# Optimization experiments

Hardware: AMD Instinct MI355X
Metric: run time of the kernel (lower is better)

## Reference

```python
import jax, jax.numpy as jnp
import numpy as np

B, S, H, W, C = 1, 42, 42, 42, 96
WS = 7            # window size (cubic)
SHIFT = 3         # cyclic shift
NH = 3            # num heads
HD = C // NH      # head dim = 32
N = WS ** 3       # tokens per window = 343
NW = (S // WS) * (H // WS) * (W // WS)  # 216 windows
SCALE = HD ** -0.5
EPS = 1e-5


def _rel_pos_index():
    # exact replica of the torch buffer construction (meshgrid 'ij')
    coords = np.stack(np.meshgrid(np.arange(WS), np.arange(WS), np.arange(WS), indexing='ij'))
    flat = coords.reshape(3, -1)                      # (3, N)
    rel = flat[:, :, None] - flat[:, None, :]          # (3, N, N)
    rel = rel.transpose(1, 2, 0).astype(np.int64)      # (N, N, 3)
    rel[..., 0] += WS - 1
    rel[..., 1] += WS - 1
    rel[..., 2] += WS - 1
    rel[..., 0] *= 3 * WS - 1
    rel[..., 1] *= 2 * WS - 1
    return jnp.asarray(rel.sum(-1))                    # (N, N) int

REL_IDX = _rel_pos_index()


def _layernorm(x, w, b):
    mu = jnp.mean(x, -1, keepdims=True)
    var = jnp.mean(jnp.square(x - mu), -1, keepdims=True)
    return (x - mu) * jax.lax.rsqrt(var + EPS) * w + b


def setup_inputs() -> dict:
    key = jax.random.key(0)
    ks = jax.random.split(key, 8)
    std = 0.02
    return {
        'x': jax.random.normal(ks[0], (B, S * H * W, C), jnp.float32),
        'mask_matrix': jnp.zeros((NW, N, N), jnp.float32),
        'norm1_w': jnp.ones((C,), jnp.float32),
        'norm1_b': jnp.zeros((C,), jnp.float32),
        'qkv_w': jax.random.normal(ks[1], (C, 3 * C), jnp.float32) * std,
        'qkv_b': jnp.zeros((3 * C,), jnp.float32),
        'proj_w': jax.random.normal(ks[2], (C, C), jnp.float32) * std,
        'proj_b': jnp.zeros((C,), jnp.float32),
        'rpb_table': jax.random.normal(ks[3], ((2 * WS - 1) ** 3, NH), jnp.float32) * std,
        'norm2_w': jnp.ones((C,), jnp.float32),
        'norm2_b': jnp.zeros((C,), jnp.float32),
        'fc1_w': jax.random.normal(ks[4], (C, 4 * C), jnp.float32) * std,
        'fc1_b': jnp.zeros((4 * C,), jnp.float32),
        'fc2_w': jax.random.normal(ks[5], (4 * C, C), jnp.float32) * std,
        'fc2_b': jnp.zeros((C,), jnp.float32),
    }


def _block(x, mask, norm1_w, norm1_b, qkv_w, qkv_b, proj_w, proj_b,
           rpb_table, norm2_w, norm2_b, fc1_w, fc1_b, fc2_w, fc2_b):
    shortcut = x
    h = _layernorm(x, norm1_w, norm1_b).reshape(B, S, H, W, C)
    # cyclic shift (S,H,W divisible by WS -> no padding needed)
    h = jnp.roll(h, shift=(-SHIFT, -SHIFT, -SHIFT), axis=(1, 2, 3))
    # window partition -> (B*nW, N, C)
    h = h.reshape(B, S // WS, WS, H // WS, WS, W // WS, WS, C)
    h = h.transpose(0, 1, 3, 5, 2, 4, 6, 7).reshape(-1, N, C)
    B_ = h.shape[0]  # B * NW
    # attention
    qkv = (h @ qkv_w + qkv_b).reshape(B_, N, 3, NH, HD).transpose(2, 0, 3, 1, 4)
    q, k, v = qkv[0] * SCALE, qkv[1], qkv[2]
    attn = jnp.einsum('bhnd,bhmd->bhnm', q, k)           # (B_, NH, N, N)
    bias = rpb_table[REL_IDX.reshape(-1)].reshape(N, N, NH).transpose(2, 0, 1)
    attn = attn + bias[None]
    attn = attn.reshape(B, NW, NH, N, N) + mask[None, :, None]
    attn = jax.nn.softmax(attn.reshape(B_, NH, N, N), axis=-1)
    out = jnp.einsum('bhnm,bhmd->bhnd', attn, v).transpose(0, 2, 1, 3).reshape(B_, N, C)
    out = out @ proj_w + proj_b
    # window reverse + reverse shift
    out = out.reshape(B, S // WS, H // WS, W // WS, WS, WS, WS, C)
    out = out.transpose(0, 1, 4, 2, 5, 3, 6, 7).reshape(B, S, H, W, C)
    out = jnp.roll(out, shift=(SHIFT, SHIFT, SHIFT), axis=(1, 2, 3)).reshape(B, S * H * W, C)
    x = shortcut + out
    # MLP with exact (erf) GELU, matching nn.GELU default
    m = _layernorm(x, norm2_w, norm2_b)
    m = jax.nn.gelu(m @ fc1_w + fc1_b, approximate=False) @ fc2_w + fc2_b
    return x + m


def reference(x, mask_matrix, norm1_w, norm1_b, qkv_w, qkv_b, proj_w, proj_b,
              rpb_table, norm2_w, norm2_b, fc1_w, fc1_b, fc2_w, fc2_b):
    return _block(x, mask_matrix, norm1_w, norm1_b, qkv_w, qkv_b, proj_w, proj_b,
                  rpb_table, norm2_w, norm2_b, fc1_w, fc1_b, fc2_w, fc2_b)
```

## Files before the change

### kernel.cpp

```cpp
#include <hip/hip_runtime.h>
#include <hip/hip_bf16.h>
#include <math.h>

#define SDIM 42
#define CDIM 96
#define NTOK 74088
#define NWIN 216
#define NSEQ 343
#define NTOT 7112448
#define QK_SCALE 0.17677669529663687f
#define LN_EPS 1e-5f

typedef short short8 __attribute__((ext_vector_type(8)));
typedef float f32x4 __attribute__((ext_vector_type(4)));
typedef unsigned eu4 __attribute__((ext_vector_type(4)));
union I4S8 { int4 i; short8 s; };

__device__ __forceinline__ int tok_index(int w, int n) {
    int wq = w / 36;
    int wrem = w - wq * 36;
    int wh = wrem / 6;
    int ww = wrem - wh * 6;
    int ps = n / 49;
    int prem = n - ps * 49;
    int ph = prem / 7;
    int pw = prem - ph * 7;
    int s = wq * 7 + ps + 3; if (s >= SDIM) s -= SDIM;
    int h = wh * 7 + ph + 3; if (h >= SDIM) h -= SDIM;
    int c = ww * 7 + pw + 3; if (c >= SDIM) c -= SDIM;
    return (s * SDIM + h) * SDIM + c;
}

__device__ __forceinline__ unsigned pk2(float a, float b) {
    unsigned ua = (unsigned)__bfloat16_as_ushort(__float2bfloat16(a));
    unsigned ub = (unsigned)__bfloat16_as_ushort(__float2bfloat16(b));
    return ua | (ub << 16);
}

__device__ __forceinline__ float fast_erf(float x) {
    float ax = fabsf(x);
    float t = 1.0f / (1.0f + 0.3275911f * ax);
    float y = t*(0.254829592f + t*(-0.284496736f +
              t*(1.421413741f + t*(-1.453152027f + t*1.061405429f))));
    float r = 1.0f - y * __expf(-ax*ax);
    return copysignf(r, x);
}
__device__ __forceinline__ float gelu(float v) {
    return 0.5f * v * (1.0f + fast_erf(v * 0.70710678118654752f));
}

__global__ __launch_bounds__(384) void k_wcast(
    const float* __restrict__ w1, const float* __restrict__ w2,
    const float* __restrict__ pw, const float* __restrict__ qkvw,
    __hip_bfloat16* __restrict__ w1t, __hip_bfloat16* __restrict__ w2t,
    __hip_bfloat16* __restrict__ pwt, __hip_bfloat16* __restrict__ qkvt)
{
    int b = blockIdx.x, t = threadIdx.x;
    if (b < 384) {
        if (t < 96) w1t[(size_t)b*96 + t] = __float2bfloat16(w1[(size_t)t*384 + b]);
    } else if (b < 480) {
        int r = b - 384;
        w2t[(size_t)r*384 + t] = __float2bfloat16(w2[(size_t)t*96 + r]);
    } else if (b < 576) {
        int r = b - 480;
        if (t < 96) pwt[(size_t)r*96 + t] = __float2bfloat16(pw[(size_t)t*96 + r]);
    } else {
        int c = b - 576;
        if (t < 96) qkvt[(size_t)c*96 + t] = __float2bfloat16(qkvw[(size_t)t*288 + c]);
    }
}

__global__ __launch_bounds__(256) void k_fused_prep(
    const float* __restrict__ x,
    const float* __restrict__ n1w, const float* __restrict__ n1b,
    const __hip_bfloat16* __restrict__ qkvt, const float* __restrict__ qkvb,
    __hip_bfloat16* __restrict__ qb, __hip_bfloat16* __restrict__ kb,
    __hip_bfloat16* __restrict__ vb,
    const float* __restrict__ mask, unsigned* __restrict__ mflag,
    const float* __restrict__ rpb, float* __restrict__ bg)
{
    __shared__ __align__(16) __hip_bfloat16 sX[64*104];
    __shared__ unsigned sFlag;
    const int b = blockIdx.x;
    const int tid = threadIdx.x;

    if (b >= 1296 + NWIN) {
        const int p = b - (1296 + NWIN);
        const int m = p % NSEQ, hh = p / NSEQ;
        const int a0 = m / 49, ar = m - a0*49, a1 = ar / 7, a2 = ar - a1*7;
        for (int n = tid; n < NSEQ; n += 256) {
            int b0 = n / 49, br = n - b0*49, b1 = br / 7, b2 = br - b1*7;
            int idx = (a0 - b0 + 6)*20 + (a1 - b1 + 6)*13 + (a2 - b2 + 6);
            bg[((size_t)hh*NSEQ + m)*NSEQ + n] = rpb[idx*3 + hh];
        }
        return;
    }
    if (b >= 1296) {
        const int w = b - 1296;
        if (tid == 0) sFlag = 0;
        __syncthreads();
        const unsigned* p = (const unsigned*)(mask + (size_t)w * NSEQ * NSEQ);
        unsigned acc = 0;
        const eu4* p4 = (const eu4*)p;
        for (int i = tid; i < (NSEQ*NSEQ)/4; i += 256) {
            eu4 v = __builtin_nontemporal_load(p4 + i);
            acc |= (v[0] << 1) | (v[1] << 1) | (v[2] << 1) | (v[3] << 1);
        }
        if (tid == 0) acc |= (p[NSEQ*NSEQ - 1] << 1);
        if (__any(acc != 0) && (tid & 63) == 0) atomicOr(&sFlag, 1u);
        __syncthreads();
        if (tid == 0) mflag[w] = sFlag;
        return;
    }

    const int w  = b / 6;
    const int n0 = (b - w*6) * 64;
    const int g = tid >> 5, l = tid & 31;
    {
        const float lw0 = n1w[l], lw1 = n1w[l+32], lw2 = n1w[l+64];
        const float lb0 = n1b[l], lb1 = n1b[l+32], lb2 = n1b[l+64];
        for (int rr = 0; rr < 8; ++rr) {
            int row = g * 8 + rr;
            int n = n0 + row;
            if (n < NSEQ) {
                const float* xr = x + (size_t)tok_index(w, n) * CDIM;
                float x0 = __builtin_nontemporal_load(xr + l);
                float x1 = __builtin_nontemporal_load(xr + l + 32);
                float x2 = __builtin_nontemporal_load(xr + l + 64);
                float s = x0 + x1 + x2;
                #pragma unroll
                for (int m = 16; m; m >>= 1) s += __shfl_xor(s, m, 32);
                float mu = s * (1.0f/96.0f);
                float d0 = x0-mu, d1 = x1-mu, d2 = x2-mu;
                float vv = d0*d0 + d1*d1 + d2*d2;
                #pragma unroll
                for (int m = 16; m; m >>= 1) vv += __shfl_xor(vv, m, 32);
                float rstd = rsqrtf(vv * (1.0f/96.0f) + LN_EPS);
                sX[row*104 + l]    = __float2bfloat16(d0 * rstd * lw0 + lb0);
                sX[row*104 + l+32] = __float2bfloat16(d1 * rstd * lw1 + lb1);
                sX[row*104 + l+64] = __float2bfloat16(d2 * rstd * lw2 + lb2);
            } else {
                sX[row*104 + l]    = __float2bfloat16(0.f);
                sX[row*104 + l+32] = __float2bfloat16(0.f);
                sX[row*104 + l+64] = __float2bfloat16(0.f);
            }
        }
    }
    __syncthreads();

    const int wv = tid >> 6, lane = tid & 63;
    const int l15 = lane & 15, h = lane >> 4;
    const int trow = wv*16 + l15;
    const int n = n0 + trow;

    I4S8 bx[3];
    #pragma unroll
    for (int ks = 0; ks < 3; ++ks)
        bx[ks].i = *(const int4*)&sX[trow*104 + ks*32 + h*8];

    for (int nt = 0; nt < 18; ++nt) {
        f32x4 acc = {0.f,0.f,0.f,0.f};
        #pragma unroll
        for (int ks = 0; ks < 3; ++ks) {
            I4S8 af;
            af.i = *(const int4*)(qkvt + (size_t)(nt*16 + l15)*96 + ks*32 + h*8);
            acc = __builtin_amdgcn_mfma_f32_16x16x32_bf16(af.s, bx[ks].s, acc, 0, 0, 0);
        }
        if (n < NSEQ) {
            const int colbase = nt*16 + 4*h;
            const int sel = colbase / 96;
            const int rem = colbase - sel*96;
            const int head = rem >> 5, d0 = rem & 31;
            float4 bb = *(const float4*)&qkvb[colbase];
            float v0 = acc[0] + bb.x, v1 = acc[1] + bb.y;
            float v2 = acc[2] + bb.z, v3 = acc[3] + bb.w;
            if (sel == 0) { v0 *= QK_SCALE; v1 *= QK_SCALE; v2 *= QK_SCALE; v3 *= QK_SCALE; }
            __hip_bfloat16* dst = (sel == 0 ? qb : (sel == 1 ? kb : vb));
            *(uint2*)&dst[(((size_t)w*3 + head)*NSEQ + n)*32 + d0] =
                make_uint2(pk2(v0, v1), pk2(v2, v3));
        }
    }
}

template<bool UM>
__device__ __forceinline__ void attn_qloop(
    const __hip_bfloat16* __restrict__ qb, const float* __restrict__ bg,
    const float* __restrict__ mask, __hip_bfloat16* __restrict__ aob,
    const __hip_bfloat16* sK, const __hip_bfloat16* sVT,
    size_t base, int w, int head, int wid, int l15, int h)
{
    for (int mt = wid; mt < 22; mt += 8) {
        const int m = mt*16 + l15;
        const int mc = (m < NSEQ) ? m : (NSEQ-1);

        I4S8 qf;
        qf.i = *(const int4*)(qb + base + (size_t)mc*32 + h*8);

        const float* mrow = mask + ((size_t)w*NSEQ + mc)*NSEQ;
        const float* brow = bg   + ((size_t)head*NSEQ + mc)*NSEQ;

        float lsum = 0.f;
        f32x4 acc0 = {0.f,0.f,0.f,0.f}, acc1 = {0.f,0.f,0.f,0.f};

        auto step = [&](int t, float4 mkA, float4 bsA, float4 mkB, float4 bsB) {
            float p[8];
            {
                I4S8 kf;
                kf.i = *(const int4*)&sK[(t*16 + l15)*32 + h*8];
                f32x4 st = __builtin_amdgcn_mfma_f32_16x16x32_bf16(
                    kf.s, qf.s, (f32x4){0.f,0.f,0.f,0.f}, 0, 0, 0);
                if constexpr (UM) {
                    p[0] = __expf(st[0] + mkA.x + bsA.x);
                    p[1] = __expf(st[1] + mkA.y + bsA.y);
                    p[2] = __expf(st[2] + mkA.z + bsA.z);
                    p[3] = __expf(st[3] + mkA.w + bsA.w);
                } else {
                    p[0] = __expf(st[0] + bsA.x);
                    p[1] = __expf(st[1] + bsA.y);
                    p[2] = __expf(st[2] + bsA.z);
                    p[3] = __expf(st[3] + bsA.w);
                }
                lsum += (p[0] + p[1]) + (p[2] + p[3]);
            }
            {
                I4S8 kf;
                kf.i = *(const int4*)&sK[((t+1)*16 + l15)*32 + h*8];
                f32x4 st = __builtin_amdgcn_mfma_f32_16x16x32_bf16(
                    kf.s, qf.s, (f32x4){0.f,0.f,0.f,0.f}, 0, 0, 0);
                if constexpr (UM) {
                    p[4] = __expf(st[0] + mkB.x + bsB.x);
                    p[5] = __expf(st[1] + mkB.y + bsB.y);
                    p[6] = __expf(st[2] + mkB.z + bsB.z);
                    p[7] = __expf(st[3] + mkB.w + bsB.w);
                } else {
                    p[4] = __expf(st[0] + bsB.x);
                    p[5] = __expf(st[1] + bsB.y);
                    p[6] = __expf(st[2] + bsB.z);
                    p[7] = __expf(st[3] + bsB.w);
                }
                lsum += (p[4] + p[5]) + (p[6] + p[7]);
            }
            I4S8 pf;
            pf.i = make_int4(pk2(p[0], p[1]), pk2(p[2], p[3]),
                             pk2(p[4], p[5]), pk2(p[6], p[7]));
            const int vcol = t*16 + 4*h;
            uint2 va0 = *(const uint2*)&sVT[(l15     )*372 + vcol];
            uint2 vb0 = *(const uint2*)&sVT[(l15     )*372 + vcol + 16];
            uint2 va1 = *(const uint2*)&sVT[(16 + l15)*372 + vcol];
            uint2 vb1 = *(const uint2*)&sVT[(16 + l15)*372 + vcol + 16];
            I4S8 vf0; vf0.i = make_int4(va0.x, va0.y, vb0.x, vb0.y);
            I4S8 vf1; vf1.i = make_int4(va1.x, va1.y, vb1.x, vb1.y);
            acc0 = __builtin_amdgcn_mfma_f32_16x16x32_bf16(vf0.s, pf.s, acc0, 0, 0, 0);
            acc1 = __builtin_amdgcn_mfma_f32_16x16x32_bf16(vf1.s, pf.s, acc1, 0, 0, 0);
        };

        const float4 z4 = {0.f,0.f,0.f,0.f};
        float4 mkA = UM ? *(const float4*)&mrow[4*h]      : z4;
        float4 bsA =      *(const float4*)&brow[4*h];
        float4 mkB = UM ? *(const float4*)&mrow[16 + 4*h] : z4;
        float4 bsB =      *(const float4*)&brow[16 + 4*h];

        #pragma unroll 1
        for (int c = 0; c < 9; ++c) {
            const int nb = (2*c + 2)*16 + 4*h;
            float4 nmkA = UM ? *(const float4*)&mrow[nb]      : z4;
            float4 nbsA =      *(const float4*)&brow[nb];
            float4 nmkB = UM ? *(const float4*)&mrow[nb + 16] : z4;
            float4 nbsB =      *(const float4*)&brow[nb + 16];
            step(2*c, mkA, bsA, mkB, bsB);
            mkA = nmkA; bsA = nbsA; mkB = nmkB; bsB = nbsB;
        }

        {
            float4 nmkA = UM ? *(const float4*)&mrow[320 + 4*h] : z4;
            float4 nbsA =      *(const float4*)&brow[320 + 4*h];
            float4 nmkB = z4, nbsB;
            {
                const int nb = 336 + 4*h;
                int i0 = nb,   c0 = (i0 < NSEQ) ? i0 : (NSEQ-1);
                int i1 = nb+1, c1 = (i1 < NSEQ) ? i1 : (NSEQ-1);
                int i2 = nb+2, c2 = (i2 < NSEQ) ? i2 : (NSEQ-1);
                int i3 = nb+3, c3 = (i3 < NSEQ) ? i3 : (NSEQ-1);
                if constexpr (UM) {
                    nmkB.x = mrow[c0]; nmkB.y = mrow[c1];
                    nmkB.z = mrow[c2]; nmkB.w = mrow[c3];
                }
                nbsB.x = brow[c0]; nbsB.y = brow[c1];
                nbsB.z = brow[c2]; nbsB.w = brow[c3];
            }
            step(18, mkA, bsA, mkB, bsB);
            mkA = nmkA; bsA = nbsA; mkB = nmkB; bsB = nbsB;
        }

        {
            float p[8];
            {
                I4S8 kf;
                kf.i = *(const int4*)&sK[(20*16 + l15)*32 + h*8];
                f32x4 st = __builtin_amdgcn_mfma_f32_16x16x32_bf16(
                    kf.s, qf.s, (f32x4){0.f,0.f,0.f,0.f}, 0, 0, 0);
                if constexpr (UM) {
                    p[0] = __expf(st[0] + mkA.x + bsA.x);
                    p[1] = __expf(st[1] + mkA.y + bsA.y);
                    p[2] = __expf(st[2] + mkA.z + bsA.z);
                    p[3] = __expf(st[3] + mkA.w + bsA.w);
                } else {
                    p[0] = __expf(st[0] + bsA.x);
                    p[1] = __expf(st[1] + bsA.y);
                    p[2] = __expf(st[2] + bsA.z);
                    p[3] = __expf(st[3] + bsA.w);
                }
                lsum += (p[0] + p[1]) + (p[2] + p[3]);
            }
            {
                I4S8 kf;
                kf.i = *(const int4*)&sK[(21*16 + l15)*32 + h*8];
                f32x4 st = __builtin_amdgcn_mfma_f32_16x16x32_bf16(
                    kf.s, qf.s, (f32x4){0.f,0.f,0.f,0.f}, 0, 0, 0);
                float sb[4];
                if constexpr (UM) {
                    sb[0] = mkB.x + bsB.x; sb[1] = mkB.y + bsB.y;
                    sb[2] = mkB.z + bsB.z; sb[3] = mkB.w + bsB.w;
                } else {
                    sb[0] = bsB.x; sb[1] = bsB.y; sb[2] = bsB.z; sb[3] = bsB.w;
                }
                const int nb = 336 + 4*h;
                #pragma unroll
                for (int r = 0; r < 4; ++r) {
                    const int nn = nb + r;
                    float e = 0.f;
                    if (nn < NSEQ) e = __expf(st[r] + sb[r]);
                    p[4+r] = e; lsum += e;
                }
            }
            I4S8 pf;
            pf.i = make_int4(pk2(p[0], p[1]), pk2(p[2], p[3]),
                             pk2(p[4], p[5]), pk2(p[6], p[7]));
            const int vcol = 320 + 4*h;
            uint2 va0 = *(const uint2*)&sVT[(l15     )*372 + vcol];
            uint2 vb0 = *(const uint2*)&sVT[(l15     )*372 + vcol + 16];
            uint2 va1 = *(const uint2*)&sVT[(16 + l15)*372 + vcol];
            uint2 vb1 = *(const uint2*)&sVT[(16 + l15)*372 + vcol + 16];
            I4S8 vf0; vf0.i = make_int4(va0.x, va0.y, vb0.x, vb0.y);
            I4S8 vf1; vf1.i = make_int4(va1.x, va1.y, vb1.x, vb1.y);
            acc0 = __builtin_amdgcn_mfma_f32_16x16x32_bf16(vf0.s, pf.s, acc0, 0, 0, 0);
            acc1 = __builtin_amdgcn_mfma_f32_16x16x32_bf16(vf1.s, pf.s, acc1, 0, 0, 0);
        }

        lsum += __shfl_xor(lsum, 16, 64);
        lsum += __shfl_xor(lsum, 32, 64);
        const float inv = 1.0f / lsum;

        if (m < NSEQ) {
            __hip_bfloat16* orow = &aob[((size_t)w*NSEQ + m)*CDIM + head*32];
            *(uint2*)&orow[4*h] =
                make_uint2(pk2(acc0[0]*inv, acc0[1]*inv), pk2(acc0[2]*inv, acc0[3]*inv));
            *(uint2*)&orow[16 + 4*h] =
                make_uint2(pk2(acc1[0]*inv, acc1[1]*inv), pk2(acc1[2]*inv, acc1[3]*inv));
        }
    }
}

__global__ __launch_bounds__(512) void k_attn(
    const __hip_bfloat16* __restrict__ qb, const __hip_bfloat16* __restrict__ kb,
    const __hip_bfloat16* __restrict__ vb, const float* __restrict__ bg,
    const float* __restrict__ mask, const unsigned* __restrict__ mflag,
    __hip_bfloat16* __restrict__ aob)
{
    __shared__ __hip_bfloat16 sK[352*32];
    __shared__ __hip_bfloat16 sVT[32*372];
    const int tid = threadIdx.x;
    const int v = blockIdx.x;
    const int xcd = v & 7, tt = v >> 3;
    const int j = tt / 3, head = tt - 3*j;
    const int w = xcd + 8*j;
    const size_t base = ((size_t)w*3 + head) * (NSEQ*32);

    {
        const int4* ksrc = (const int4*)(kb + base);
        for (int i = tid; i < NSEQ*4; i += 512) {
            int row = i >> 2, q = i & 3;
            *(int4*)&sK[row*32 + q*8] = ksrc[i];
        }
        const int4* vsrc = (const int4*)(vb + base);
        for (int i = tid; i < NSEQ*4; i += 512) {
            int n = i >> 2, dc = i & 3;
            int4 t = vsrc[i];
            const __hip_bfloat16* tp = (const __hip_bfloat16*)&t;
            #pragma unroll
            for (int k2 = 0; k2 < 8; ++k2) sVT[(dc*8 + k2)*372 + n] = tp[k2];
        }
        for (int i = tid; i < 32*29; i += 512) {
            int d = i / 29, n = NSEQ + (i - d*29);
            sVT[d*372 + n] = __float2bfloat16(0.f);
        }
    }
    __syncthreads();

    const int wid = tid >> 6, lane = tid & 63;
    const int l15 = lane & 15, h = lane >> 4;

    if (mflag[w] == 0)
        attn_qloop<false>(qb, bg, mask, aob, sK, sVT, base, w, head, wid, l15, h);
    else
        attn_qloop<true>(qb, bg, mask, aob, sK, sVT, base, w, head, wid, l15, h);
}

__global__ __launch_bounds__(256) void k_pmlp(
    const __hip_bfloat16* __restrict__ aob, const __hip_bfloat16* __restrict__ pwt,
    const float* __restrict__ pb, const float* __restrict__ x,
    const float* __restrict__ n2w, const float* __restrict__ n2b,
    const __hip_bfloat16* __restrict__ w1t, const float* __restrict__ b1,
    const __hip_bfloat16* __restrict__ w2t, const float* __restrict__ b2,
    float* __restrict__ out)
{
    __shared__ __align__(16) __hip_bfloat16 sBuf[64*104];
    __shared__ __align__(16) __hip_bfloat16 sW[96*100];
    const int w = blockIdx.y;
    const int n0 = blockIdx.x * 64;
    const int tid = threadIdx.x;
    const int wv = tid >> 6, lane = tid & 63;
    const int l15 = lane & 15, h = lane >> 4;
    const int trow = wv*16 + l15;
    const int n = n0 + trow;
    const int nc = (n < NSEQ) ? n : (NSEQ-1);
    const int tok = tok_index(w, nc);

    for (int i = tid; i < 1152; i += 256) {
        int row = i / 12, cb = i - row*12;
        int4 t = *(const int4*)(pwt + (size_t)row*96 + cb*8);
        *(int4*)&sW[row*100 + cb*8] = t;
    }
    I4S8 bm[3];
    #pragma unroll
    for (int ks = 0; ks < 3; ++ks)
        bm[ks].i = *(const int4*)(aob + ((size_t)w*NSEQ + nc)*CDIM + ks*32 + h*8);
    __syncthreads();

    float4 x1v[6];
    #pragma unroll
    for (int nt = 0; nt < 6; ++nt) {
        f32x4 acc = {0.f,0.f,0.f,0.f};
        #pragma unroll
        for (int ks = 0; ks < 3; ++ks) {
            I4S8 af;
            af.i = *(const int4*)&sW[(nt*16 + l15)*100 + ks*32 + h*8];
            acc = __builtin_amdgcn_mfma_f32_16x16x32_bf16(af.s, bm[ks].s, acc, 0, 0, 0);
        }
        const int col = nt*16 + 4*h;
        float4 xr = *(const float4*)&x[(size_t)tok*CDIM + col];
        float4 bb = *(const float4*)&pb[col];
        x1v[nt].x = xr.x + acc[0] + bb.x;
        x1v[nt].y = xr.y + acc[1] + bb.y;
        x1v[nt].z = xr.z + acc[2] + bb.z;
        x1v[nt].w = xr.w + acc[3] + bb.w;
    }

    {
        float s = 0.f, q = 0.f;
        #pragma unroll
        for (int nt = 0; nt < 6; ++nt) {
            s += (x1v[nt].x + x1v[nt].y) + (x1v[nt].z + x1v[nt].w);
            q += (x1v[nt].x*x1v[nt].x + x1v[nt].y*x1v[nt].y)
               + (x1v[nt].z*x1v[nt].z + x1v[nt].w*x1v[nt].w);
        }
        s += __shfl_xor(s, 16, 64); s += __shfl_xor(s, 32, 64);
        q += __shfl_xor(q, 16, 64); q += __shfl_xor(q, 32, 64);
        float mu = s * (1.0f/96.0f);
        float var = q * (1.0f/96.0f) - mu*mu;
        float rstd = rsqrtf(var + LN_EPS);
        #pragma unroll
        for (int nt = 0; nt < 6; ++nt) {
            const int col = nt*16 + 4*h;
            float4 nwv = *(const float4*)&n2w[col];
            float4 nbv = *(const float4*)&n2b[col];
            float a0 = (x1v[nt].x - mu)*rstd*nwv.x + nbv.x;
            float a1 = (x1v[nt].y - mu)*rstd*nwv.y + nbv.y;
            float a2 = (x1v[nt].z - mu)*rstd*nwv.z + nbv.z;
            float a3 = (x1v[nt].w - mu)*rstd*nwv.w + nbv.w;
            *(uint2*)&sBuf[trow*104 + col] = make_uint2(pk2(a0, a1), pk2(a2, a3));
        }
    }

    I4S8 bx[3];
    #pragma unroll
    for (int ks = 0; ks < 3; ++ks)
        bx[ks].i = *(const int4*)&sBuf[trow*104 + ks*32 + h*8];

    f32x4 accs[6];
    #pragma unroll
    for (int nt = 0; nt < 6; ++nt) accs[nt] = (f32x4){0.f,0.f,0.f,0.f};

    #pragma unroll 1
    for (int q = 0; q < 4; ++q) {
        __syncthreads();
        for (int i = tid; i < 1152; i += 256) {
            int row = i / 12, cb = i - row*12;
            int4 t = *(const int4*)(w1t + (size_t)(q*96 + row)*96 + cb*8);
            *(int4*)&sW[row*100 + cb*8] = t;
        }
        __syncthreads();

        #pragma unroll
        for (int ntl = 0; ntl < 6; ++ntl) {
            I4S8 af[3];
            #pragma unroll
            for (int ks = 0; ks < 3; ++ks)
                af[ks].i = *(const int4*)&sW[(ntl*16 + l15)*100 + ks*32 + h*8];
            f32x4 acc = {0.f,0.f,0.f,0.f};
            #pragma unroll
            for (int ks = 0; ks < 3; ++ks)
                acc = __builtin_amdgcn_mfma_f32_16x16x32_bf16(af[ks].s, bx[ks].s, acc, 0, 0, 0);
            float4 bb = *(const float4*)&b1[q*96 + ntl*16 + 4*h];
            *(uint2*)&sBuf[trow*104 + ntl*16 + 4*h] =
                make_uint2(pk2(gelu(acc[0]+bb.x), gelu(acc[1]+bb.y)),
                           pk2(gelu(acc[2]+bb.z), gelu(acc[3]+bb.w)));
        }

        __syncthreads();
        for (int i = tid; i < 1152; i += 256) {
            int row = i / 12, cb = i - row*12;
            int4 t = *(const int4*)(w2t + (size_t)row*384 + q*96 + cb*8);
            *(int4*)&sW[row*100 + cb*8] = t;
        }
        __syncthreads();

        #pragma unroll
        for (int ksl = 0; ksl < 3; ++ksl) {
            I4S8 bmq;
            bmq.i = *(const int4*)&sBuf[trow*104 + ksl*32 + h*8];
            #pragma unroll
            for (int nt = 0; nt < 6; ++nt) {
                I4S8 af;
                af.i = *(const int4*)&sW[(nt*16 + l15)*100 + ksl*32 + h*8];
                accs[nt] = __builtin_amdgcn_mfma_f32_16x16x32_bf16(af.s, bmq.s, accs[nt], 0, 0, 0);
            }
        }
    }

    if (n < NSEQ) {
        #pragma unroll
        for (int nt = 0; nt < 6; ++nt) {
            const int col = nt*16 + 4*h;
            float4 bb = *(const float4*)&b2[col];
            float4 o;
            o.x = x1v[nt].x + accs[nt][0] + bb.x;
            o.y = x1v[nt].y + accs[nt][1] + bb.y;
            o.z = x1v[nt].z + accs[nt][2] + bb.z;
            o.w = x1v[nt].w + accs[nt][3] + bb.w;
            *(float4*)&out[(size_t)tok*CDIM + col] = o;
        }
    }
}

extern "C" void kernel_launch(void* const* d_in, const int* in_sizes, int n_in,
                              void* d_out, int out_size, void* d_ws, size_t ws_size,
                              hipStream_t stream) {
    const float* x    = (const float*)d_in[0];
    const float* mask = (const float*)d_in[1];
    const float* n1w  = (const float*)d_in[2];
    const float* n1b  = (const float*)d_in[3];
    const float* qkvw = (const float*)d_in[4];
    const float* qkvb = (const float*)d_in[5];
    const float* pw   = (const float*)d_in[6];
    const float* pb   = (const float*)d_in[7];
    const float* rpb  = (const float*)d_in[8];
    const float* n2w  = (const float*)d_in[9];
    const float* n2b  = (const float*)d_in[10];
    const float* w1   = (const float*)d_in[11];
    const float* b1   = (const float*)d_in[12];
    const float* w2   = (const float*)d_in[13];
    const float* b2   = (const float*)d_in[14];
    float* out = (float*)d_out;

    __hip_bfloat16* qb  = (__hip_bfloat16*)d_ws;
    __hip_bfloat16* kb  = qb + NTOT;
    __hip_bfloat16* vb  = kb + NTOT;
    __hip_bfloat16* aob = vb + NTOT;
    float* bg = (float*)(aob + NTOT);
    __hip_bfloat16* w1t  = (__hip_bfloat16*)(bg + 352948);
    __hip_bfloat16* w2t  = w1t + 384*96;
    __hip_bfloat16* pwt  = w2t + 96*384;
    __hip_bfloat16* qkvt = pwt + 96*96;
    unsigned* mflag = (unsigned*)(qkvt + 288*96);

    hipLaunchKernelGGL(k_wcast, dim3(864), dim3(384), 0, stream,
                       w1, w2, pw, qkvw, w1t, w2t, pwt, qkvt);
    hipLaunchKernelGGL(k_fused_prep, dim3(1296 + NWIN + NSEQ*3), dim3(256), 0, stream,
                       x, n1w, n1b, qkvt, qkvb, qb, kb, vb, mask, mflag, rpb, bg);
    hipLaunchKernelGGL(k_attn, dim3(NWIN*3), dim3(512), 0, stream,
                       qb, kb, vb, bg, mask, mflag, aob);
    hipLaunchKernelGGL(k_pmlp, dim3(6, NWIN), dim3(256), 0, stream,
                       aob, pwt, pb, x, n2w, n2b, w1t, b1, w2t, b2, out);
}
```

Before: 191.0 us.

## Double-buffer MLP weight staging via registers and split mask scan into quarters

The projection+MLP kernel now prefetches the next weight tile from global memory into registers while the current tile is consumed from a second shared-memory buffer. This halves the barriers per iteration and hides global load latency behind MFMA work. The mask-flag scan is split across four blocks per window, using a global atomicOr on a flag zeroed in the weight-cast kernel, to add parallelism. The cost is more shared memory and registers per block, which may lower occupancy.

Measured after the change: 164.6 us, median of 4. -13.8%, faster.

```diff
diff --git a/kernel.cpp b/kernel.cpp
--- a/kernel.cpp
+++ b/kernel.cpp
@@ -53,7 +53,8 @@
     const float* __restrict__ w1, const float* __restrict__ w2,
     const float* __restrict__ pw, const float* __restrict__ qkvw,
     __hip_bfloat16* __restrict__ w1t, __hip_bfloat16* __restrict__ w2t,
-    __hip_bfloat16* __restrict__ pwt, __hip_bfloat16* __restrict__ qkvt)
+    __hip_bfloat16* __restrict__ pwt, __hip_bfloat16* __restrict__ qkvt,
+    unsigned* __restrict__ mflag)
 {
     int b = blockIdx.x, t = threadIdx.x;
     if (b < 384) {
@@ -64,9 +65,11 @@
     } else if (b < 576) {
         int r = b - 480;
         if (t < 96) pwt[(size_t)r*96 + t] = __float2bfloat16(pw[(size_t)t*96 + r]);
-    } else {
+    } else if (b < 864) {
         int c = b - 576;
         if (t < 96) qkvt[(size_t)c*96 + t] = __float2bfloat16(qkvw[(size_t)t*288 + c]);
+    } else {
+        if (t < NWIN) mflag[t] = 0;
     }
 }
 
@@ -80,12 +83,11 @@
     const float* __restrict__ rpb, float* __restrict__ bg)
 {
     __shared__ __align__(16) __hip_bfloat16 sX[64*104];
-    __shared__ unsigned sFlag;
     const int b = blockIdx.x;
     const int tid = threadIdx.x;
 
-    if (b >= 1296 + NWIN) {
-        const int p = b - (1296 + NWIN);
+    if (b >= 2160) {
+        const int p = b - 2160;
         const int m = p % NSEQ, hh = p / NSEQ;
         const int a0 = m / 49, ar = m - a0*49, a1 = ar / 7, a2 = ar - a1*7;
         for (int n = tid; n < NSEQ; n += 256) {
@@ -96,20 +98,18 @@
         return;
     }
     if (b >= 1296) {
-        const int w = b - 1296;
-        if (tid == 0) sFlag = 0;
-        __syncthreads();
+        const int idx = b - 1296;
+        const int w = idx >> 2, part = idx & 3;
         const unsigned* p = (const unsigned*)(mask + (size_t)w * NSEQ * NSEQ);
+        const eu4* p4 = (const eu4*)p;
         unsigned acc = 0;
-        const eu4* p4 = (const eu4*)p;
-        for (int i = tid; i < (NSEQ*NSEQ)/4; i += 256) {
+        const int lo = part * 7353, hi = lo + 7353;
+        for (int i = lo + tid; i < hi; i += 256) {
             eu4 v = __builtin_nontemporal_load(p4 + i);
             acc |= (v[0] << 1) | (v[1] << 1) | (v[2] << 1) | (v[3] << 1);
         }
-        if (tid == 0) acc |= (p[NSEQ*NSEQ - 1] << 1);
-        if (__any(acc != 0) && (tid & 63) == 0) atomicOr(&sFlag, 1u);
-        __syncthreads();
-        if (tid == 0) mflag[w] = sFlag;
+        if (part == 3 && tid == 0) acc |= (p[NSEQ*NSEQ - 1] << 1);
+        if (__any(acc != 0) && (tid & 63) == 0) atomicOr(&mflag[w], 1u);
         return;
     }
 
@@ -415,7 +415,7 @@
     float* __restrict__ out)
 {
     __shared__ __align__(16) __hip_bfloat16 sBuf[64*104];
-    __shared__ __align__(16) __hip_bfloat16 sW[96*100];
+    __shared__ __align__(16) __hip_bfloat16 sW[2][96*100];
     const int w = blockIdx.y;
     const int n0 = blockIdx.x * 64;
     const int tid = threadIdx.x;
@@ -426,17 +426,33 @@
     const int nc = (n < NSEQ) ? n : (NSEQ-1);
     const int tok = tok_index(w, nc);
 
-    for (int i = tid; i < 1152; i += 256) {
-        int row = i / 12, cb = i - row*12;
-        int4 t = *(const int4*)(pwt + (size_t)row*96 + cb*8);
-        *(int4*)&sW[row*100 + cb*8] = t;
-    }
+    uint2 st[9];
+    auto stage_load = [&](const __hip_bfloat16* src, int stride) {
+        #pragma unroll
+        for (int r = 0; r < 9; ++r) {
+            int i = tid + r*256;
+            int row = i / 24, cb = i - row*24;
+            st[r] = *(const uint2*)(src + (size_t)row*stride + cb*4);
+        }
+    };
+    auto stage_write = [&](int buf) {
+        #pragma unroll
+        for (int r = 0; r < 9; ++r) {
+            int i = tid + r*256;
+            int row = i / 24, cb = i - row*24;
+            *(uint2*)&sW[buf][row*100 + cb*4] = st[r];
+        }
+    };
+
+    stage_load(pwt, 96);
     I4S8 bm[3];
     #pragma unroll
     for (int ks = 0; ks < 3; ++ks)
         bm[ks].i = *(const int4*)(aob + ((size_t)w*NSEQ + nc)*CDIM + ks*32 + h*8);
+    stage_write(0);
     __syncthreads();
 
+    stage_load(w1t, 96);
     float4 x1v[6];
     #pragma unroll
     for (int nt = 0; nt < 6; ++nt) {
@@ -444,7 +460,7 @@
         #pragma unroll
         for (int ks = 0; ks < 3; ++ks) {
             I4S8 af;
-            af.i = *(const int4*)&sW[(nt*16 + l15)*100 + ks*32 + h*8];
+            af.i = *(const int4*)&sW[0][(nt*16 + l15)*100 + ks*32 + h*8];
             acc = __builtin_amdgcn_mfma_f32_16x16x32_bf16(af.s, bm[ks].s, acc, 0, 0, 0);
         }
         const int col = nt*16 + 4*h;
@@ -455,7 +471,6 @@
         x1v[nt].z = xr.z + acc[2] + bb.z;
         x1v[nt].w = xr.w + acc[3] + bb.w;
     }
-
     {
         float s = 0.f, q = 0.f;
         #pragma unroll
@@ -481,11 +496,12 @@
             *(uint2*)&sBuf[trow*104 + col] = make_uint2(pk2(a0, a1), pk2(a2, a3));
         }
     }
-
     I4S8 bx[3];
     #pragma unroll
     for (int ks = 0; ks < 3; ++ks)
         bx[ks].i = *(const int4*)&sBuf[trow*104 + ks*32 + h*8];
+    stage_write(1);
+    __syncthreads();
 
     f32x4 accs[6];
     #pragma unroll
@@ -493,20 +509,13 @@
 
     #pragma unroll 1
     for (int q = 0; q < 4; ++q) {
-        __syncthreads();
-        for (int i = tid; i < 1152; i += 256) {
-            int row = i / 12, cb = i - row*12;
-            int4 t = *(const int4*)(w1t + (size_t)(q*96 + row)*96 + cb*8);
-            *(int4*)&sW[row*100 + cb*8] = t;
-        }
-        __syncthreads();
-
+        stage_load(w2t + q*96, 384);
         #pragma unroll
         for (int ntl = 0; ntl < 6; ++ntl) {
             I4S8 af[3];
             #pragma unroll
             for (int ks = 0; ks < 3; ++ks)
-                af[ks].i = *(const int4*)&sW[(ntl*16 + l15)*100 + ks*32 + h*8];
+                af[ks].i = *(const int4*)&sW[1][(ntl*16 + l15)*100 + ks*32 + h*8];
             f32x4 acc = {0.f,0.f,0.f,0.f};
             #pragma unroll
             for (int ks = 0; ks < 3; ++ks)
@@ -516,15 +525,10 @@
                 make_uint2(pk2(gelu(acc[0]+bb.x), gelu(acc[1]+bb.y)),
                            pk2(gelu(acc[2]+bb.z), gelu(acc[3]+bb.w)));
         }
-
+        stage_write(0);
         __syncthreads();
-        for (int i = tid; i < 1152; i += 256) {
-            int row = i / 12, cb = i - row*12;
-            int4 t = *(const int4*)(w2t + (size_t)row*384 + q*96 + cb*8);
-            *(int4*)&sW[row*100 + cb*8] = t;
-        }
-        __syncthreads();
-
+
+        if (q < 3) stage_load(w1t + (size_t)(q+1)*96*96, 96);
         #pragma unroll
         for (int ksl = 0; ksl < 3; ++ksl) {
             I4S8 bmq;
@@ -532,9 +536,13 @@
             #pragma unroll
             for (int nt = 0; nt < 6; ++nt) {
                 I4S8 af;
-                af.i = *(const int4*)&sW[(nt*16 + l15)*100 + ksl*32 + h*8];
+                af.i = *(const int4*)&sW[0][(nt*16 + l15)*100 + ksl*32 + h*8];
                 accs[nt] = __builtin_amdgcn_mfma_f32_16x16x32_bf16(af.s, bmq.s, accs[nt], 0, 0, 0);
             }
+        }
+        if (q < 3) {
+            stage_write(1);
+            __syncthreads();
         }
     }
 
@@ -584,9 +592,9 @@
     __hip_bfloat16* qkvt = pwt + 96*96;
     unsigned* mflag = (unsigned*)(qkvt + 288*96);
 
-    hipLaunchKernelGGL(k_wcast, dim3(864), dim3(384), 0, stream,
-                       w1, w2, pw, qkvw, w1t, w2t, pwt, qkvt);
-    hipLaunchKernelGGL(k_fused_prep, dim3(1296 + NWIN + NSEQ*3), dim3(256), 0, stream,
+    hipLaunchKernelGGL(k_wcast, dim3(865), dim3(384), 0, stream,
+                       w1, w2, pw, qkvw, w1t, w2t, pwt, qkvt, mflag);
+    hipLaunchKernelGGL(k_fused_prep, dim3(1296 + 4*NWIN + NSEQ*3), dim3(256), 0, stream,
                        x, n1w, n1b, qkvt, qkvb, qb, kb, vb, mask, mflag, rpb, bg);
     hipLaunchKernelGGL(k_attn, dim3(NWIN*3), dim3(512), 0, stream,
                        qb, kb, vb, bg, mask, mflag, aob);
```
